# Optimization experiments

Hardware: AMD Instinct MI355X
Metric: run time of the kernel (lower is better)

The kernel has to match this reference:

```python
import jax, jax.numpy as jnp
import numpy as np

INPUT_DIM, LATENT_DIM, HIDDEN_DIM, BATCH = 1024, 128, 1024, 32768


def setup_inputs() -> dict:
    key = jax.random.key(0)
    ks = jax.random.split(key, 12)
    s = 0.02
    x = (jax.random.uniform(ks[0], (BATCH, INPUT_DIM)) < 0.5).astype(jnp.float32)  # binary data
    eps = jax.random.normal(ks[1], (BATCH, LATENT_DIM), dtype=jnp.float32)
    return {
        "x": x,
        "eps": eps,
        "We1": jax.random.normal(ks[2], (INPUT_DIM, HIDDEN_DIM)) * s,
        "be1": jnp.zeros((HIDDEN_DIM,), jnp.float32),
        "Wmu": jax.random.normal(ks[3], (HIDDEN_DIM, LATENT_DIM)) * s,
        "bmu": jnp.zeros((LATENT_DIM,), jnp.float32),
        "Wls": jax.random.normal(ks[4], (HIDDEN_DIM, LATENT_DIM)) * s,
        "bls": jnp.zeros((LATENT_DIM,), jnp.float32),
        "Wd1": jax.random.normal(ks[5], (LATENT_DIM, HIDDEN_DIM)) * s,
        "bd1": jnp.zeros((HIDDEN_DIM,), jnp.float32),
        "Wd2": jax.random.normal(ks[6], (HIDDEN_DIM, INPUT_DIM)) * s,
        "bd2": jnp.zeros((INPUT_DIM,), jnp.float32),
    }


def reference(x, eps, We1, be1, Wmu, bmu, Wls, bls, Wd1, bd1, Wd2, bd2):
    # Encoder: one hidden ReLU layer, mu / logsigma heads
    h = jax.nn.relu(x @ We1 + be1)                      # [B, H]
    mu = h @ Wmu + bmu                                  # [B, L]
    logsigma = h @ Wls + bls                            # [B, L]
    # Reparameterization: z = sigma * eps + mu (vectorized diag(exp(logsigma)) @ eps)
    z = mu + jnp.exp(logsigma) * eps                    # [B, L]
    # Decoder: one hidden ReLU layer, sigmoid Bernoulli params
    hd = jax.nn.relu(z @ Wd1 + bd1)                     # [B, H]
    theta = jax.nn.sigmoid(hd @ Wd2 + bd2)              # [B, D]
    # Bernoulli log-likelihood: sum_j log(theta^x * (1-theta)^(1-x))
    log_px = jnp.sum(x * jnp.log(theta) + (1.0 - x) * jnp.log1p(-theta), axis=-1)  # [B]
    # KL(q||N(0,I)) = 0.5 * sum(sigma^2 + mu^2 - log(sigma^2) - 1)
    kl = 0.5 * jnp.sum(jnp.exp(2.0 * logsigma) + mu * mu - 2.0 * logsigma - 1.0, axis=-1)  # [B]
    return log_px - kl                                  # elbo_mc [B]
```

## Files before the change

### kernel.cpp

```cpp
#include <hip/hip_runtime.h>
#include <cstdint>
#include <cstddef>


typedef __bf16 bf16x8 __attribute__((ext_vector_type(8)));
typedef float f32x4 __attribute__((ext_vector_type(4)));

__device__ __forceinline__ unsigned short f32_to_bf16(float f) {
  unsigned int u = __float_as_uint(f);
  u += 0x7fffu + ((u >> 16) & 1u);
  return (unsigned short)(u >> 16);
}

struct TransJob { const float* in; unsigned short* out; int K, N, blkEnd; };

__global__ void prep_k(TransJob j0, TransJob j1, TransJob j2, TransJob j3,
                       TransJob j4, const float* __restrict__ x,
                       unsigned short* __restrict__ xbf, int n4) {
  int bid = blockIdx.x;
  int tid = threadIdx.y * 32 + threadIdx.x;
  if (bid >= 2432) {
    int base = (bid - 2432) * 256 + tid;
    int stride = 2048 * 256;
#pragma unroll
    for (int it = 0; it < 16; ++it) {
      int i = base + it * stride;
      float4 v = reinterpret_cast<const float4*>(x)[i];
      ushort4 o = make_ushort4(f32_to_bf16(v.x), f32_to_bf16(v.y),
                               f32_to_bf16(v.z), f32_to_bf16(v.w));
      reinterpret_cast<ushort4*>(xbf)[i] = o;
    }
    return;
  }
  __shared__ float tile[32][33];
  TransJob j; int base;
  if (bid < j0.blkEnd)      { j = j0; base = 0; }
  else if (bid < j1.blkEnd) { j = j1; base = j0.blkEnd; }
  else if (bid < j2.blkEnd) { j = j2; base = j1.blkEnd; }
  else if (bid < j3.blkEnd) { j = j3; base = j2.blkEnd; }
  else                      { j = j4; base = j3.blkEnd; }
  int local = bid - base;
  int gxN = j.N >> 5;
  int n0 = (local % gxN) * 32, k0 = (local / gxN) * 32;
  int tx = threadIdx.x, ty = threadIdx.y;
#pragma unroll
  for (int r = 0; r < 32; r += 8)
    tile[ty + r][tx] = j.in[(size_t)(k0 + ty + r) * j.N + n0 + tx];
  __syncthreads();
#pragma unroll
  for (int r = 0; r < 32; r += 8)
    j.out[(size_t)(n0 + ty + r) * j.K + k0 + tx] = f32_to_bf16(tile[tx][ty + r]);
}

__device__ __forceinline__ void gl_lds16(const unsigned short* g, unsigned short* l) {
  __builtin_amdgcn_global_load_lds(
      (__attribute__((address_space(1))) void*)g,
      (__attribute__((address_space(3))) void*)l, 16, 0, 0);
}

template <int EPI>
__global__ __launch_bounds__(256) void gemm_bt(
    const unsigned short* __restrict__ A, const unsigned short* __restrict__ BT,
    int gx, int N, int K,
    const float* __restrict__ bias0,
    unsigned short* __restrict__ outb, float* __restrict__ outf,
    const unsigned short* __restrict__ xbf) {
  __shared__ __align__(16) unsigned short As[2][128 * 32];
  __shared__ __align__(16) unsigned short Bs[2][128 * 32];

  const int tid = threadIdx.x;
  const int lane = tid & 63;
  const int wave = tid >> 6;
  const int wr = wave >> 1, wc = wave & 1;
  const int bid = blockIdx.x;
  const int xcd = bid & 7;
  const int t8 = bid >> 3;
  const int m0 = (xcd + 8 * (t8 / gx)) * 128;
  const int n0 = (t8 % gx) * 128;
  const int lm = lane & 15, lq = lane >> 4;

  const int c0 = tid, c1 = tid + 256;
  const int row0 = c0 >> 2, q0 = (c0 & 3) ^ ((row0 >> 1) & 3);
  const int row1 = c1 >> 2, q1 = (c1 & 3) ^ ((row1 >> 1) & 3);
  const unsigned short* agp0 = A + (size_t)(m0 + row0) * K + q0 * 8;
  const unsigned short* agp1 = A + (size_t)(m0 + row1) * K + q1 * 8;
  const unsigned short* bgp0 = BT + (size_t)(n0 + row0) * K + q0 * 8;
  const unsigned short* bgp1 = BT + (size_t)(n0 + row1) * K + q1 * 8;

  const int so = (lq ^ ((lm >> 1) & 3)) * 8;

  f32x4 acc[4][4] = {};
  const int nIter = K >> 5;

  gl_lds16(agp0, As[0] + c0 * 8);
  gl_lds16(agp1, As[0] + c1 * 8);
  gl_lds16(bgp0, Bs[0] + c0 * 8);
  gl_lds16(bgp1, Bs[0] + c1 * 8);
  __syncthreads();

  for (int it = 0; it < nIter; ++it) {
    const int p = it & 1;
    if (it + 1 < nIter) {
      const int off = (it + 1) << 5;
      gl_lds16(agp0 + off, As[1 - p] + c0 * 8);
      gl_lds16(agp1 + off, As[1 - p] + c1 * 8);
      gl_lds16(bgp0 + off, Bs[1 - p] + c0 * 8);
      gl_lds16(bgp1 + off, Bs[1 - p] + c1 * 8);
    }

    bf16x8 af[4], bfr[4];
#pragma unroll
    for (int i = 0; i < 4; ++i)
      af[i] = *reinterpret_cast<const bf16x8*>(As[p] + (wr * 64 + i * 16 + lm) * 32 + so);
#pragma unroll
    for (int j = 0; j < 4; ++j)
      bfr[j] = *reinterpret_cast<const bf16x8*>(Bs[p] + (wc * 64 + j * 16 + lm) * 32 + so);
#pragma unroll
    for (int i = 0; i < 4; ++i)
#pragma unroll
      for (int j = 0; j < 4; ++j)
        acc[i][j] = __builtin_amdgcn_mfma_f32_16x16x32_bf16(af[i], bfr[j], acc[i][j], 0, 0, 0);
    __syncthreads();
  }

  if (EPI == 0) {
#pragma unroll
    for (int i = 0; i < 4; ++i)
#pragma unroll
      for (int j = 0; j < 4; ++j) {
        int col = n0 + wc * 64 + j * 16 + lm;
        float bias = bias0[col];
#pragma unroll
        for (int r = 0; r < 4; ++r) {
          int row = m0 + wr * 64 + i * 16 + lq * 4 + r;
          float v = acc[i][j][r] + bias;
          v = fmaxf(v, 0.f);
          outb[(size_t)row * N + col] = f32_to_bf16(v);
        }
      }
  } else {
#pragma unroll
    for (int i = 0; i < 4; ++i) {
      float rs[4] = {0.f, 0.f, 0.f, 0.f};
#pragma unroll
      for (int j = 0; j < 4; ++j) {
        int col = n0 + wc * 64 + j * 16 + lm;
        float bias = bias0[col];
#pragma unroll
        for (int r = 0; r < 4; ++r) {
          int row = m0 + wr * 64 + i * 16 + lq * 4 + r;
          float l = acc[i][j][r] + bias;
          unsigned short xb = xbf[(size_t)row * N + col];
          float t = xb ? -l : l;
          float sp = fmaxf(t, 0.f) + __logf(1.f + __expf(-fabsf(t)));
          rs[r] -= sp;
        }
      }
#pragma unroll
      for (int off = 1; off < 16; off <<= 1)
#pragma unroll
        for (int r = 0; r < 4; ++r) rs[r] += __shfl_xor(rs[r], off, 64);
      if (lm == 0) {
#pragma unroll
        for (int r = 0; r < 4; ++r)
          atomicAdd(&outf[m0 + wr * 64 + i * 16 + lq * 4 + r], rs[r]);
      }
    }
  }
}

__global__ __launch_bounds__(256) void gemm23_zkl(
    const unsigned short* __restrict__ A,
    const unsigned short* __restrict__ BT,
    const unsigned short* __restrict__ WD1,
    const float* __restrict__ bmu, const float* __restrict__ bls,
    const float* __restrict__ bd1,
    const float* __restrict__ eps,
    unsigned short* __restrict__ hd,
    float* __restrict__ out) {
  __shared__ __align__(16) unsigned short lds[24576];
  unsigned short* As = lds;
  unsigned short* Bs = lds + 4096;
  unsigned short* zs = lds;
  unsigned short* Ws = lds + 8192;

  const int tid = threadIdx.x;
  const int lane = tid & 63;
  const int wave = tid >> 6;
  const int m0 = blockIdx.x * 64;
  const int lm = lane & 15, lq = lane >> 4;
  const int K = 1024;

  const unsigned short* agp[2];
  const unsigned short* bgp[8];
#pragma unroll
  for (int r = 0; r < 2; ++r) {
    int c = tid + 256 * r;
    int row = c >> 3, q = (c & 7) ^ (row & 7);
    agp[r] = A + (size_t)(m0 + row) * K + q * 8;
  }
#pragma unroll
  for (int r = 0; r < 8; ++r) {
    int c = tid + 256 * r;
    int row = c >> 3, q = (c & 7) ^ (row & 7);
    bgp[r] = BT + (size_t)row * K + q * 8;
  }
  const int sw = lm & 7;

  f32x4 acc[16] = {};

  for (int kt = 0; kt < K; kt += 64) {
#pragma unroll
    for (int r = 0; r < 2; ++r) gl_lds16(agp[r] + kt, As + (tid + 256 * r) * 8);
#pragma unroll
    for (int r = 0; r < 8; ++r) gl_lds16(bgp[r] + kt, Bs + (tid + 256 * r) * 8);
    __syncthreads();

#pragma unroll
    for (int s = 0; s < 2; ++s) {
      const int so = ((s << 2) | lq) ^ sw;
      bf16x8 af = *reinterpret_cast<const bf16x8*>(As + (wave * 16 + lm) * 64 + so * 8);
#pragma unroll
      for (int j = 0; j < 16; ++j) {
        bf16x8 b = *reinterpret_cast<const bf16x8*>(Bs + (j * 16 + lm) * 64 + so * 8);
        acc[j] = __builtin_amdgcn_mfma_f32_16x16x32_bf16(af, b, acc[j], 0, 0, 0);
      }
    }
    __syncthreads();
  }

  float kl[4] = {0.f, 0.f, 0.f, 0.f};
#pragma unroll
  for (int j = 0; j < 8; ++j) {
    int dim = j * 16 + lm;
    float bm = bmu[dim], bl = bls[dim];
    int chunk = dim >> 3;
#pragma unroll
    for (int r = 0; r < 4; ++r) {
      int lr = wave * 16 + lq * 4 + r;
      float mu = acc[j][r] + bm;
      float ls = acc[j + 8][r] + bl;
      float e = eps[(size_t)(m0 + lr) * 128 + dim];
      float zz = fmaf(__expf(ls), e, mu);
      int slot = chunk ^ (lr & 15);
      zs[lr * 128 + slot * 8 + (dim & 7)] = f32_to_bf16(zz);
      kl[r] += 0.5f * (__expf(2.f * ls) + mu * mu - 2.f * ls - 1.f);
    }
  }
#pragma unroll
  for (int off = 1; off < 16; off <<= 1)
#pragma unroll
    for (int r = 0; r < 4; ++r) kl[r] += __shfl_xor(kl[r], off, 64);
  if (lm == 0) {
#pragma unroll
    for (int r = 0; r < 4; ++r)
      out[m0 + wave * 16 + lq * 4 + r] = -kl[r];
  }

  int wrow[8], wq[8];
#pragma unroll
  for (int r = 0; r < 8; ++r) {
    int c = tid + 256 * r;
    wrow[r] = c >> 4;
    wq[r] = (c & 15) ^ (wrow[r] & 15);
  }

  for (int cc = 0; cc < 8; ++cc) {
#pragma unroll
    for (int r = 0; r < 8; ++r)
      gl_lds16(WD1 + (size_t)(cc * 128 + wrow[r]) * 128 + wq[r] * 8,
               Ws + (tid + 256 * r) * 8);
    __syncthreads();

    f32x4 acc2[4][2] = {};
#pragma unroll
    for (int s = 0; s < 4; ++s) {
      const int c = (s << 2) | lq;
      const int so = c ^ lm;
      bf16x8 af[4];
#pragma unroll
      for (int it = 0; it < 4; ++it)
        af[it] = *reinterpret_cast<const bf16x8*>(zs + (it * 16 + lm) * 128 + so * 8);
#pragma unroll
      for (int jt = 0; jt < 2; ++jt) {
        bf16x8 b = *reinterpret_cast<const bf16x8*>(
            Ws + (wave * 32 + jt * 16 + lm) * 128 + so * 8);
#pragma unroll
        for (int it = 0; it < 4; ++it)
          acc2[it][jt] = __builtin_amdgcn_mfma_f32_16x16x32_bf16(af[it], b, acc2[it][jt], 0, 0, 0);
      }
    }
    __syncthreads();

#pragma unroll
    for (int jt = 0; jt < 2; ++jt) {
      int col = cc * 128 + wave * 32 + jt * 16 + lm;
      float bias = bd1[col];
#pragma unroll
      for (int it = 0; it < 4; ++it)
#pragma unroll
        for (int r = 0; r < 4; ++r) {
          int row = m0 + it * 16 + lq * 4 + r;
          float v = acc2[it][jt][r] + bias;
          v = fmaxf(v, 0.f);
          hd[(size_t)row * 1024 + col] = f32_to_bf16(v);
        }
    }
  }
}

extern "C" void kernel_launch(void* const* d_in, const int* in_sizes, int n_in,
                              void* d_out, int out_size, void* d_ws, size_t ws_size,
                              hipStream_t stream) {
  const float* x   = (const float*)d_in[0];
  const float* eps = (const float*)d_in[1];
  const float* We1 = (const float*)d_in[2];
  const float* be1 = (const float*)d_in[3];
  const float* Wmu = (const float*)d_in[4];
  const float* bmu = (const float*)d_in[5];
  const float* Wls = (const float*)d_in[6];
  const float* bls = (const float*)d_in[7];
  const float* Wd1 = (const float*)d_in[8];
  const float* bd1 = (const float*)d_in[9];
  const float* Wd2 = (const float*)d_in[10];
  const float* bd2 = (const float*)d_in[11];
  float* out = (float*)d_out;

  const int B = 32768, D = 1024, H = 1024, L = 128;

  char* ws = (char*)d_ws;
  size_t off = 0;
  auto alloc = [&](size_t bytes) {
    void* p = ws + off;
    off += (bytes + 255) & ~(size_t)255;
    return p;
  };
  unsigned short* xbf  = (unsigned short*)alloc((size_t)B * D * 2);
  unsigned short* w1t  = (unsigned short*)alloc((size_t)H * D * 2);
  unsigned short* w2t  = (unsigned short*)alloc((size_t)256 * H * 2);
  unsigned short* wd1t = (unsigned short*)alloc((size_t)H * L * 2);
  unsigned short* wd2t = (unsigned short*)alloc((size_t)D * H * 2);
  unsigned short* h    = (unsigned short*)alloc((size_t)B * H * 2);
  unsigned short* hd   = h;

  TransJob j0{We1, w1t, D, H, 1024};
  TransJob j1{Wmu, w2t, H, L, 1152};
  TransJob j2{Wls, w2t + 128 * H, H, L, 1280};
  TransJob j3{Wd1, wd1t, L, H, 1408};
  TransJob j4{Wd2, wd2t, H, D, 2432};
  prep_k<<<4480, dim3(32, 8), 0, stream>>>(j0, j1, j2, j3, j4, x, xbf, B * D / 4);

  gemm_bt<0><<<8 * 256, 256, 0, stream>>>(
      xbf, w1t, 8, H, D, be1, h, nullptr, nullptr);
  gemm23_zkl<<<B / 64, 256, 0, stream>>>(h, w2t, wd1t, bmu, bls, bd1, eps, hd, out);
  gemm_bt<2><<<8 * 256, 256, 0, stream>>>(
      hd, wd2t, 8, D, H, bd2, nullptr, out, xbf);

  (void)in_sizes; (void)n_in; (void)out_size; (void)ws_size;
}
```

Measured before the change: 473.3 us.

## Switch all GEMMs and intermediates from bf16 to fp8 MFMA with new LDS layouts

Converts the weights, the binary input x and the hidden activations to fp8 (e4m3) rather than bf16, and uses the fp8 16x16x32 MFMA in all three GEMM kernels. LDS tiles are re-laid out into 16-byte half-K slabs with 8-byte fragment reads, which replaces the earlier XOR swizzles. This halves the memory traffic for the intermediates and doubles the peak MFMA rate. In exchange, fp8 quantization of the weights, the hidden activations and z lowers accuracy, and the new LDS layout may add bank conflicts.

```diff
diff --git a/kernel.cpp b/kernel.cpp
--- a/kernel.cpp
+++ b/kernel.cpp
@@ -3,20 +3,32 @@
 #include <cstddef>
 
 
-typedef __bf16 bf16x8 __attribute__((ext_vector_type(8)));
 typedef float f32x4 __attribute__((ext_vector_type(4)));
 
-__device__ __forceinline__ unsigned short f32_to_bf16(float f) {
-  unsigned int u = __float_as_uint(f);
-  u += 0x7fffu + ((u >> 16) & 1u);
-  return (unsigned short)(u >> 16);
-}
-
-struct TransJob { const float* in; unsigned short* out; int K, N, blkEnd; };
+__device__ __forceinline__ unsigned char f32_to_fp8(float f) {
+#if __has_builtin(__builtin_amdgcn_cvt_pk_fp8_f32)
+  return (unsigned char)(__builtin_amdgcn_cvt_pk_fp8_f32(f, 0.f, 0, false) & 0xff);
+#else
+  unsigned u = __float_as_uint(f);
+  unsigned s = (u >> 24) & 0x80u;
+  float a = fabsf(f);
+  if (!(a < 448.f)) return (unsigned char)(s | 0x7E);
+  if (a < 0.015625f) {
+    int m = (int)rintf(a * 512.f);
+    return (unsigned char)(s | (m == 8 ? 0x08 : m));
+  }
+  int e; float mant = frexpf(a, &e);
+  int m = (int)rintf(mant * 16.f);
+  if (m >= 16) { m = 8; e += 1; }
+  return (unsigned char)(s | ((unsigned)(e - 1 + 7) << 3) | (unsigned)(m & 7));
+#endif
+}
+
+struct TransJob { const float* in; unsigned char* out; int K, N, blkEnd; };
 
 __global__ void prep_k(TransJob j0, TransJob j1, TransJob j2, TransJob j3,
                        TransJob j4, const float* __restrict__ x,
-                       unsigned short* __restrict__ xbf, int n4) {
+                       unsigned char* __restrict__ xq) {
   int bid = blockIdx.x;
   int tid = threadIdx.y * 32 + threadIdx.x;
   if (bid >= 2432) {
@@ -26,9 +38,9 @@
     for (int it = 0; it < 16; ++it) {
       int i = base + it * stride;
       float4 v = reinterpret_cast<const float4*>(x)[i];
-      ushort4 o = make_ushort4(f32_to_bf16(v.x), f32_to_bf16(v.y),
-                               f32_to_bf16(v.z), f32_to_bf16(v.w));
-      reinterpret_cast<ushort4*>(xbf)[i] = o;
+      uchar4 o = make_uchar4(v.x != 0.f ? 0x38 : 0, v.y != 0.f ? 0x38 : 0,
+                             v.z != 0.f ? 0x38 : 0, v.w != 0.f ? 0x38 : 0);
+      reinterpret_cast<uchar4*>(xq)[i] = o;
     }
     return;
   }
@@ -49,10 +61,10 @@
   __syncthreads();
 #pragma unroll
   for (int r = 0; r < 32; r += 8)
-    j.out[(size_t)(n0 + ty + r) * j.K + k0 + tx] = f32_to_bf16(tile[tx][ty + r]);
-}
-
-__device__ __forceinline__ void gl_lds16(const unsigned short* g, unsigned short* l) {
+    j.out[(size_t)(n0 + ty + r) * j.K + k0 + tx] = f32_to_fp8(tile[tx][ty + r]);
+}
+
+__device__ __forceinline__ void gl_lds16(const unsigned char* g, unsigned char* l) {
   __builtin_amdgcn_global_load_lds(
       (__attribute__((address_space(1))) void*)g,
       (__attribute__((address_space(3))) void*)l, 16, 0, 0);
@@ -60,13 +72,13 @@
 
 template <int EPI>
 __global__ __launch_bounds__(256) void gemm_bt(
-    const unsigned short* __restrict__ A, const unsigned short* __restrict__ BT,
+    const unsigned char* __restrict__ A, const unsigned char* __restrict__ BT,
     int gx, int N, int K,
     const float* __restrict__ bias0,
-    unsigned short* __restrict__ outb, float* __restrict__ outf,
-    const unsigned short* __restrict__ xbf) {
-  __shared__ __align__(16) unsigned short As[2][128 * 32];
-  __shared__ __align__(16) unsigned short Bs[2][128 * 32];
+    unsigned char* __restrict__ outb, float* __restrict__ outf,
+    const unsigned char* __restrict__ xq) {
+  __shared__ __align__(16) unsigned char As[2][128 * 32];
+  __shared__ __align__(16) unsigned char Bs[2][128 * 32];
 
   const int tid = threadIdx.x;
   const int lane = tid & 63;
@@ -79,47 +91,39 @@
   const int n0 = (t8 % gx) * 128;
   const int lm = lane & 15, lq = lane >> 4;
 
-  const int c0 = tid, c1 = tid + 256;
-  const int row0 = c0 >> 2, q0 = (c0 & 3) ^ ((row0 >> 1) & 3);
-  const int row1 = c1 >> 2, q1 = (c1 & 3) ^ ((row1 >> 1) & 3);
-  const unsigned short* agp0 = A + (size_t)(m0 + row0) * K + q0 * 8;
-  const unsigned short* agp1 = A + (size_t)(m0 + row1) * K + q1 * 8;
-  const unsigned short* bgp0 = BT + (size_t)(n0 + row0) * K + q0 * 8;
-  const unsigned short* bgp1 = BT + (size_t)(n0 + row1) * K + q1 * 8;
-
-  const int so = (lq ^ ((lm >> 1) & 3)) * 8;
+  const int hh = tid >> 7, rr = tid & 127;
+  const unsigned char* agp = A + (size_t)(m0 + rr) * K + hh * 16;
+  const unsigned char* bgp = BT + (size_t)(n0 + rr) * K + hh * 16;
+
+  const int rdo = (lq >> 1) * 2048 + (lq & 1) * 8;
 
   f32x4 acc[4][4] = {};
   const int nIter = K >> 5;
 
-  gl_lds16(agp0, As[0] + c0 * 8);
-  gl_lds16(agp1, As[0] + c1 * 8);
-  gl_lds16(bgp0, Bs[0] + c0 * 8);
-  gl_lds16(bgp1, Bs[0] + c1 * 8);
+  gl_lds16(agp, As[0] + tid * 16);
+  gl_lds16(bgp, Bs[0] + tid * 16);
   __syncthreads();
 
   for (int it = 0; it < nIter; ++it) {
     const int p = it & 1;
     if (it + 1 < nIter) {
       const int off = (it + 1) << 5;
-      gl_lds16(agp0 + off, As[1 - p] + c0 * 8);
-      gl_lds16(agp1 + off, As[1 - p] + c1 * 8);
-      gl_lds16(bgp0 + off, Bs[1 - p] + c0 * 8);
-      gl_lds16(bgp1 + off, Bs[1 - p] + c1 * 8);
-    }
-
-    bf16x8 af[4], bfr[4];
+      gl_lds16(agp + off, As[1 - p] + tid * 16);
+      gl_lds16(bgp + off, Bs[1 - p] + tid * 16);
+    }
+
+    long long af[4], bfr[4];
 #pragma unroll
     for (int i = 0; i < 4; ++i)
-      af[i] = *reinterpret_cast<const bf16x8*>(As[p] + (wr * 64 + i * 16 + lm) * 32 + so);
+      af[i] = *reinterpret_cast<const long long*>(As[p] + rdo + (wr * 64 + i * 16 + lm) * 16);
 #pragma unroll
     for (int j = 0; j < 4; ++j)
-      bfr[j] = *reinterpret_cast<const bf16x8*>(Bs[p] + (wc * 64 + j * 16 + lm) * 32 + so);
+      bfr[j] = *reinterpret_cast<const long long*>(Bs[p] + rdo + (wc * 64 + j * 16 + lm) * 16);
 #pragma unroll
     for (int i = 0; i < 4; ++i)
 #pragma unroll
       for (int j = 0; j < 4; ++j)
-        acc[i][j] = __builtin_amdgcn_mfma_f32_16x16x32_bf16(af[i], bfr[j], acc[i][j], 0, 0, 0);
+        acc[i][j] = __builtin_amdgcn_mfma_f32_16x16x32_fp8_fp8(af[i], bfr[j], acc[i][j], 0, 0, 0);
     __syncthreads();
   }
 
@@ -135,7 +139,7 @@
           int row = m0 + wr * 64 + i * 16 + lq * 4 + r;
           float v = acc[i][j][r] + bias;
           v = fmaxf(v, 0.f);
-          outb[(size_t)row * N + col] = f32_to_bf16(v);
+          outb[(size_t)row * N + col] = f32_to_fp8(v);
         }
       }
   } else {
@@ -150,7 +154,7 @@
         for (int r = 0; r < 4; ++r) {
           int row = m0 + wr * 64 + i * 16 + lq * 4 + r;
           float l = acc[i][j][r] + bias;
-          unsigned short xb = xbf[(size_t)row * N + col];
+          unsigned char xb = xq[(size_t)row * N + col];
           float t = xb ? -l : l;
           float sp = fmaxf(t, 0.f) + __logf(1.f + __expf(-fabsf(t)));
           rs[r] -= sp;
@@ -170,19 +174,19 @@
 }
 
 __global__ __launch_bounds__(256) void gemm23_zkl(
-    const unsigned short* __restrict__ A,
-    const unsigned short* __restrict__ BT,
-    const unsigned short* __restrict__ WD1,
+    const unsigned char* __restrict__ A,
+    const unsigned char* __restrict__ BT,
+    const unsigned char* __restrict__ WD1,
     const float* __restrict__ bmu, const float* __restrict__ bls,
     const float* __restrict__ bd1,
     const float* __restrict__ eps,
-    unsigned short* __restrict__ hd,
+    unsigned char* __restrict__ hd,
     float* __restrict__ out) {
-  __shared__ __align__(16) unsigned short lds[24576];
-  unsigned short* As = lds;
-  unsigned short* Bs = lds + 4096;
-  unsigned short* zs = lds;
-  unsigned short* Ws = lds + 8192;
+  __shared__ __align__(16) unsigned char lds[24576];
+  unsigned char* As = lds;
+  unsigned char* Bs = lds + 4096;
+  unsigned char* zs = lds;
+  unsigned char* Ws = lds + 8192;
 
   const int tid = threadIdx.x;
   const int lane = tid & 63;
@@ -191,39 +195,30 @@
   const int lm = lane & 15, lq = lane >> 4;
   const int K = 1024;
 
-  const unsigned short* agp[2];
-  const unsigned short* bgp[8];
-#pragma unroll
-  for (int r = 0; r < 2; ++r) {
-    int c = tid + 256 * r;
-    int row = c >> 3, q = (c & 7) ^ (row & 7);
-    agp[r] = A + (size_t)(m0 + row) * K + q * 8;
-  }
-#pragma unroll
-  for (int r = 0; r < 8; ++r) {
-    int c = tid + 256 * r;
-    int row = c >> 3, q = (c & 7) ^ (row & 7);
-    bgp[r] = BT + (size_t)row * K + q * 8;
-  }
-  const int sw = lm & 7;
+  const int ah = tid >> 6, ar = tid & 63;
+  const unsigned char* agp = A + (size_t)(m0 + ar) * K + ah * 16;
+  const unsigned char* bgp = BT + (size_t)tid * K;
 
   f32x4 acc[16] = {};
 
   for (int kt = 0; kt < K; kt += 64) {
-#pragma unroll
-    for (int r = 0; r < 2; ++r) gl_lds16(agp[r] + kt, As + (tid + 256 * r) * 8);
-#pragma unroll
-    for (int r = 0; r < 8; ++r) gl_lds16(bgp[r] + kt, Bs + (tid + 256 * r) * 8);
+    gl_lds16(agp + kt, As + tid * 16);
+#pragma unroll
+    for (int r = 0; r < 4; ++r)
+      gl_lds16(bgp + kt + r * 16, Bs + (r * 256 + tid) * 16);
     __syncthreads();
 
 #pragma unroll
     for (int s = 0; s < 2; ++s) {
-      const int so = ((s << 2) | lq) ^ sw;
-      bf16x8 af = *reinterpret_cast<const bf16x8*>(As + (wave * 16 + lm) * 64 + so * 8);
+      const int h = s * 2 + (lq >> 1);
+      const int bo = (lq & 1) * 8;
+      long long af = *reinterpret_cast<const long long*>(
+          As + h * 1024 + (wave * 16 + lm) * 16 + bo);
 #pragma unroll
       for (int j = 0; j < 16; ++j) {
-        bf16x8 b = *reinterpret_cast<const bf16x8*>(Bs + (j * 16 + lm) * 64 + so * 8);
-        acc[j] = __builtin_amdgcn_mfma_f32_16x16x32_bf16(af, b, acc[j], 0, 0, 0);
+        long long b = *reinterpret_cast<const long long*>(
+            Bs + h * 4096 + (j * 16 + lm) * 16 + bo);
+        acc[j] = __builtin_amdgcn_mfma_f32_16x16x32_fp8_fp8(af, b, acc[j], 0, 0, 0);
       }
     }
     __syncthreads();
@@ -234,7 +229,6 @@
   for (int j = 0; j < 8; ++j) {
     int dim = j * 16 + lm;
     float bm = bmu[dim], bl = bls[dim];
-    int chunk = dim >> 3;
 #pragma unroll
     for (int r = 0; r < 4; ++r) {
       int lr = wave * 16 + lq * 4 + r;
@@ -242,8 +236,7 @@
       float ls = acc[j + 8][r] + bl;
       float e = eps[(size_t)(m0 + lr) * 128 + dim];
       float zz = fmaf(__expf(ls), e, mu);
-      int slot = chunk ^ (lr & 15);
-      zs[lr * 128 + slot * 8 + (dim & 7)] = f32_to_bf16(zz);
+      zs[j * 1024 + lr * 16 + lm] = f32_to_fp8(zz);
       kl[r] += 0.5f * (__expf(2.f * ls) + mu * mu - 2.f * ls - 1.f);
     }
   }
@@ -257,37 +250,32 @@
       out[m0 + wave * 16 + lq * 4 + r] = -kl[r];
   }
 
-  int wrow[8], wq[8];
-#pragma unroll
-  for (int r = 0; r < 8; ++r) {
-    int c = tid + 256 * r;
-    wrow[r] = c >> 4;
-    wq[r] = (c & 15) ^ (wrow[r] & 15);
-  }
-
   for (int cc = 0; cc < 8; ++cc) {
 #pragma unroll
-    for (int r = 0; r < 8; ++r)
-      gl_lds16(WD1 + (size_t)(cc * 128 + wrow[r]) * 128 + wq[r] * 8,
-               Ws + (tid + 256 * r) * 8);
+    for (int r = 0; r < 4; ++r) {
+      int sc = r * 256 + tid;
+      int h = sc >> 7, wrow = sc & 127;
+      gl_lds16(WD1 + (size_t)(cc * 128 + wrow) * 128 + h * 16, Ws + sc * 16);
+    }
     __syncthreads();
 
     f32x4 acc2[4][2] = {};
 #pragma unroll
     for (int s = 0; s < 4; ++s) {
-      const int c = (s << 2) | lq;
-      const int so = c ^ lm;
-      bf16x8 af[4];
+      const int h = s * 2 + (lq >> 1);
+      const int bo = (lq & 1) * 8;
+      long long af[4];
 #pragma unroll
       for (int it = 0; it < 4; ++it)
-        af[it] = *reinterpret_cast<const bf16x8*>(zs + (it * 16 + lm) * 128 + so * 8);
+        af[it] = *reinterpret_cast<const long long*>(
+            zs + h * 1024 + (it * 16 + lm) * 16 + bo);
 #pragma unroll
       for (int jt = 0; jt < 2; ++jt) {
-        bf16x8 b = *reinterpret_cast<const bf16x8*>(
-            Ws + (wave * 32 + jt * 16 + lm) * 128 + so * 8);
+        long long b = *reinterpret_cast<const long long*>(
+            Ws + h * 2048 + (wave * 32 + jt * 16 + lm) * 16 + bo);
 #pragma unroll
         for (int it = 0; it < 4; ++it)
-          acc2[it][jt] = __builtin_amdgcn_mfma_f32_16x16x32_bf16(af[it], b, acc2[it][jt], 0, 0, 0);
+          acc2[it][jt] = __builtin_amdgcn_mfma_f32_16x16x32_fp8_fp8(af[it], b, acc2[it][jt], 0, 0, 0);
       }
     }
     __syncthreads();
@@ -303,7 +291,7 @@
           int row = m0 + it * 16 + lq * 4 + r;
           float v = acc2[it][jt][r] + bias;
           v = fmaxf(v, 0.f);
-          hd[(size_t)row * 1024 + col] = f32_to_bf16(v);
+          hd[(size_t)row * 1024 + col] = f32_to_fp8(v);
         }
     }
   }
@@ -335,26 +323,26 @@
     off += (bytes + 255) & ~(size_t)255;
     return p;
   };
-  unsigned short* xbf  = (unsigned short*)alloc((size_t)B * D * 2);
-  unsigned short* w1t  = (unsigned short*)alloc((size_t)H * D * 2);
-  unsigned short* w2t  = (unsigned short*)alloc((size_t)256 * H * 2);
-  unsigned short* wd1t = (unsigned short*)alloc((size_t)H * L * 2);
-  unsigned short* wd2t = (unsigned short*)alloc((size_t)D * H * 2);
-  unsigned short* h    = (unsigned short*)alloc((size_t)B * H * 2);
-  unsigned short* hd   = h;
+  unsigned char* xq   = (unsigned char*)alloc((size_t)B * D);
+  unsigned char* w1t  = (unsigned char*)alloc((size_t)H * D);
+  unsigned char* w2t  = (unsigned char*)alloc((size_t)256 * H);
+  unsigned char* wd1t = (unsigned char*)alloc((size_t)H * L);
+  unsigned char* wd2t = (unsigned char*)alloc((size_t)D * H);
+  unsigned char* h    = (unsigned char*)alloc((size_t)B * H);
+  unsigned char* hd   = h;
 
   TransJob j0{We1, w1t, D, H, 1024};
   TransJob j1{Wmu, w2t, H, L, 1152};
   TransJob j2{Wls, w2t + 128 * H, H, L, 1280};
   TransJob j3{Wd1, wd1t, L, H, 1408};
   TransJob j4{Wd2, wd2t, H, D, 2432};
-  prep_k<<<4480, dim3(32, 8), 0, stream>>>(j0, j1, j2, j3, j4, x, xbf, B * D / 4);
+  prep_k<<<4480, dim3(32, 8), 0, stream>>>(j0, j1, j2, j3, j4, x, xq);
 
   gemm_bt<0><<<8 * 256, 256, 0, stream>>>(
-      xbf, w1t, 8, H, D, be1, h, nullptr, nullptr);
+      xq, w1t, 8, H, D, be1, h, nullptr, nullptr);
   gemm23_zkl<<<B / 64, 256, 0, stream>>>(h, w2t, wd1t, bmu, bls, bd1, eps, hd, out);
   gemm_bt<2><<<8 * 256, 256, 0, stream>>>(
-      hd, wd2t, 8, D, H, bd2, nullptr, out, xbf);
+      hd, wd2t, 8, D, H, bd2, nullptr, out, xq);
 
   (void)in_sizes; (void)n_in; (void)out_size; (void)ws_size;
 }
```

New measurement: 478.9 us. About the same (+1.2%).
